# Kernel optimization log

Hardware: AMD Instinct MI355X
Metric: run time of the kernel (lower is better)

## Reference

```python
import jax, jax.numpy as jnp
import numpy as np
import itertools

D_MODEL = 1024
TEMP = 0.3


def _hypercube(n):
    # all 2^n corners of {-1,+1}^n, matching generate_hypercube(n)
    return jnp.asarray(np.array(list(itertools.product([-1.0, 1.0], repeat=n)), dtype=np.float32))


def setup_inputs() -> dict:
    key = jax.random.key(0)
    ks = jax.random.split(key, 12)
    B, T, D = 8, 4096, D_MODEL
    s = 0.02
    return {
        "x": jax.random.normal(ks[0], (B, T, D), dtype=jnp.float32),
        "codes_l1": _hypercube(3),   # (8, 3)
        "codes_l2": _hypercube(6),   # (64, 6)
        "w_to_l1": jax.random.normal(ks[1], (D, 3), dtype=jnp.float32) * s,
        "w_from_l1": jax.random.normal(ks[2], (3, D), dtype=jnp.float32) * s,
        "w_to_l2": jax.random.normal(ks[3], (D, 6), dtype=jnp.float32) * s,
        "w_from_l2": jax.random.normal(ks[4], (6, D), dtype=jnp.float32) * s,
        "w_to_l3u": jax.random.normal(ks[5], (D, 6), dtype=jnp.float32) * s,
        "w_to_l3l": jax.random.normal(ks[6], (D, 6), dtype=jnp.float32) * s,
        "w_from_l3": jax.random.normal(ks[7], (12, D), dtype=jnp.float32) * s,
        "w_gate": jax.random.normal(ks[8], (D, 3), dtype=jnp.float32) * s,
        "b_gate": jnp.zeros((3,), dtype=jnp.float32),
        "temp_l1": jnp.log(jnp.float32(TEMP)),
        "temp_l2": jnp.log(jnp.float32(TEMP * 0.7)),
        "temp_l3": jnp.log(jnp.float32(TEMP * 0.5)),
        "scale_l1": jnp.float32(0.1),
        "scale_l2": jnp.float32(0.05),
        "scale_l3": jnp.float32(0.02),
    }


def _soft_quantize(z, codes, temp_log):
    # z: (B, T, n); codes: (K, n) -> (B, T, n)
    temp = jnp.clip(jnp.exp(temp_log), 0.01, 5.0)
    # Euclidean cdist: (B, T, K)
    dists = jnp.sqrt(jnp.sum(jnp.square(z[..., None, :] - codes), axis=-1))
    weights = jax.nn.softmax(-dists / temp, axis=-1)
    return weights @ codes


def reference(x, codes_l1, codes_l2, w_to_l1, w_from_l1, w_to_l2, w_from_l2,
              w_to_l3u, w_to_l3l, w_from_l3, w_gate, b_gate,
              temp_l1, temp_l2, temp_l3, scale_l1, scale_l2, scale_l3):
    # gate uses detached x
    gate = jax.nn.softmax(jax.lax.stop_gradient(x) @ w_gate + b_gate, axis=-1)  # (B,T,3)

    # Level 1: Z2^3
    q1 = _soft_quantize(x @ w_to_l1, codes_l1, temp_l1)
    out_l1 = q1 @ w_from_l1

    # Level 2: Z2^6
    q2 = _soft_quantize(x @ w_to_l2, codes_l2, temp_l2)
    out_l2 = q2 @ w_from_l2

    # Level 3: Z2^12 = two Z2^6 halves
    q3u = _soft_quantize(x @ w_to_l3u, codes_l2, temp_l3)
    q3l = _soft_quantize(x @ w_to_l3l, codes_l2, temp_l3)
    out_l3 = jnp.concatenate([q3u, q3l], axis=-1) @ w_from_l3

    out = (gate[..., 0:1] * scale_l1 * out_l1
           + gate[..., 1:2] * scale_l2 * out_l2
           + gate[..., 2:3] * scale_l3 * out_l3)
    gate_means = jnp.mean(gate, axis=(0, 1))  # stats dict analogue: (3,)
    return x + out, gate_means
```

## Files before the change

### kernel.cpp

```cpp
#include <hip/hip_runtime.h>
#include <stdint.h>


#define DM 1024
#define TPB 64
#define OUT_OFF ((size_t)33554432)
#define NTOK 32768
#define NSLOT 32
#define WSA_OFF 32768

typedef float f32x4 __attribute__((ext_vector_type(4)));
typedef short bf16x8 __attribute__((ext_vector_type(8)));

typedef const __attribute__((address_space(1))) unsigned int* gas1_t;
typedef __attribute__((address_space(3))) unsigned int* las3_t;

__device__ __forceinline__ void gl_lds16(const void* g, void* l){
  __builtin_amdgcn_global_load_lds((gas1_t)g, (las3_t)l, 16, 0, 0);
}

__device__ __forceinline__ short f2bf(float f){
  unsigned u = __builtin_bit_cast(unsigned, f);
  unsigned r = u + 0x7fffu + ((u >> 16) & 1u);
  return (short)(r >> 16);
}

template<int NB>
__device__ __forceinline__ void softq(const float* z, float invt, float* q){
  constexpr int K = 1 << NB;
  float d[K];
  float dmin = 3.4e38f;
#pragma unroll
  for (int j = 0; j < K; ++j){
    float acc = 0.f;
#pragma unroll
    for (int i = 0; i < NB; ++i){
      float c = ((j >> (NB-1-i)) & 1) ? 1.f : -1.f;
      float t = z[i] - c;
      acc = fmaf(t, t, acc);
    }
    float dj = sqrtf(acc);
    d[j] = dj;
    dmin = fminf(dmin, dj);
  }
  float S = 0.f;
  float s1[NB];
#pragma unroll
  for (int i = 0; i < NB; ++i) s1[i] = 0.f;
#pragma unroll
  for (int j = 0; j < K; ++j){
    float wj = __expf((dmin - d[j]) * invt);
    S += wj;
#pragma unroll
    for (int i = 0; i < NB; ++i)
      if ((j >> (NB-1-i)) & 1) s1[i] += wj;
  }
  float rS = 1.f / S;
#pragma unroll
  for (int i = 0; i < NB; ++i) q[i] = 2.f * s1[i] * rS - 1.f;
}

__global__ __launch_bounds__(256) void pack_kernel(
    const float* __restrict__ w_to_l1,  const float* __restrict__ w_to_l2,
    const float* __restrict__ w_to_l3u, const float* __restrict__ w_to_l3l,
    const float* __restrict__ w_gate,
    const float* __restrict__ w_from_l1, const float* __restrict__ w_from_l2,
    const float* __restrict__ w_from_l3,
    short* __restrict__ wsF, float* __restrict__ wsA)
{
  int base = blockIdx.x*4096 + threadIdx.x*16;
#pragma unroll
  for (int q = 0; q < 16; ++q){
    int e = base + q;
    float v;
    if (e < 32768){
      int s  = e >> 10;
      int nf = (e >> 9) & 1;
      int ll = (e >> 3) & 63;
      int j  = e & 7;
      int k  = s*32 + ((ll >> 4) << 3) + j;
      int n  = nf*16 + (ll & 15);
      if      (n < 3)  v = w_gate  [k*3 + n];
      else if (n < 6)  v = w_to_l1 [k*3 + (n-3)];
      else if (n < 12) v = w_to_l2 [k*6 + (n-6)];
      else if (n < 18) v = w_to_l3u[k*6 + (n-12)];
      else if (n < 24) v = w_to_l3l[k*6 + (n-18)];
      else             v = 0.f;
    } else {
      int e2  = e - 32768;
      int f   = e2 / 384;
      int rem = e2 - f*384;
      int ll  = rem >> 3;
      int j   = e2 & 7;
      int k   = ((ll >> 4) << 3) + j;
      int dd  = f*16 + (ll & 15);
      if      (k < 3)  v = w_from_l1[k*DM + dd];
      else if (k < 9)  v = w_from_l2[(k-3)*DM + dd];
      else if (k < 21) v = w_from_l3[(k-9)*DM + dd];
      else             v = 0.f;
    }
    wsF[e] = f2bf(v);
  }
  if (blockIdx.x == 0){
    wsA[threadIdx.x]       = 0.f;
    wsA[threadIdx.x + 256] = 0.f;
  }
}

__global__ __launch_bounds__(256, 2) void hq8_kernel(
    const float* __restrict__ x, const short* __restrict__ wsF,
    const float* __restrict__ b_gate,
    const float* __restrict__ t1p, const float* __restrict__ t2p, const float* __restrict__ t3p,
    const float* __restrict__ s1p, const float* __restrict__ s2p, const float* __restrict__ s3p,
    float* __restrict__ wsA, float* __restrict__ out)
{
  __shared__ alignas(16) char smem[65536];

  const int tid  = threadIdx.x;
  const int l    = tid & 63;
  const int wv   = tid >> 6;
  const int kg   = l >> 4;
  const int ln16 = l & 15;
  const int tokBase = blockIdx.x * TPB + wv*16;

  char*  W  = smem + wv*16384;
  float* Cw = reinterpret_cast<float*>(W + 8192);
  float* Pw = reinterpret_cast<float*>(W + 12544);
  short* Vw = reinterpret_cast<short*>(W + 14720);

  const float invt1 = 1.f / fminf(fmaxf(__expf(t1p[0]), 0.01f), 5.0f);
  const float invt2 = 1.f / fminf(fmaxf(__expf(t2p[0]), 0.01f), 5.0f);
  const float invt3 = 1.f / fminf(fmaxf(__expf(t3p[0]), 0.01f), 5.0f);
  const float s1v = s1p[0], s2v = s2p[0], s3v = s3p[0];
  const float bg0 = b_gate[0], bg1 = b_gate[1], bg2 = b_gate[2];

  {
    f32x4 acc0 = {0.f,0.f,0.f,0.f}, acc1 = {0.f,0.f,0.f,0.f};
    const int lr0 = l >> 5;
    const int cbp = l & 31;
#pragma unroll
    for (int i = 0; i < 8; ++i){
      int lr = i*2 + lr0;
      gl_lds16(x + (size_t)(tokBase + lr)*DM + (cbp ^ (lr & 7))*4,
               W + i*1024 + l*16);
    }
#pragma unroll
    for (int t = 0; t < 8; ++t){
      const int buf = t & 1;
      bf16x8 bfr[8];
#pragma unroll
      for (int s2 = 0; s2 < 8; ++s2)
        bfr[s2] = *reinterpret_cast<const bf16x8*>(&wsF[(t*8 + s2)*512 + l*8]);
      __builtin_amdgcn_sched_barrier(0);
      if (t < 7){
#pragma unroll
        for (int i = 0; i < 8; ++i){
          int lr = i*2 + lr0;
          gl_lds16(x + (size_t)(tokBase + lr)*DM + (t+1)*128 + (cbp ^ (lr & 7))*4,
                   W + (buf^1)*8192 + i*1024 + l*16);
        }
        asm volatile("s_waitcnt vmcnt(8)" ::: "memory");
      } else {
        asm volatile("s_waitcnt vmcnt(0)" ::: "memory");
      }
      const char* abase = W + buf*8192 + ln16*512;
#pragma unroll
      for (int s = 0; s < 4; ++s){
        float4 xa = *reinterpret_cast<const float4*>(abase + ((s*8 + kg*2 + 0) ^ (ln16 & 7))*16);
        float4 xb = *reinterpret_cast<const float4*>(abase + ((s*8 + kg*2 + 1) ^ (ln16 & 7))*16);
        bf16x8 af;
        af[0]=f2bf(xa.x); af[1]=f2bf(xa.y); af[2]=f2bf(xa.z); af[3]=f2bf(xa.w);
        af[4]=f2bf(xb.x); af[5]=f2bf(xb.y); af[6]=f2bf(xb.z); af[7]=f2bf(xb.w);
        acc0 = __builtin_amdgcn_mfma_f32_16x16x32_bf16(af, bfr[s*2+0], acc0, 0, 0, 0);
        acc1 = __builtin_amdgcn_mfma_f32_16x16x32_bf16(af, bfr[s*2+1], acc1, 0, 0, 0);
      }
    }
#pragma unroll
    for (int r = 0; r < 4; ++r){
      int row = kg*4 + r;
      Pw[row*34 + ln16]      = acc0[r];
      Pw[row*34 + 16 + ln16] = acc1[r];
    }
  }

  const short* wsFC = wsF + 32768;
  bf16x8 bwc0={0,0,0,0,0,0,0,0}, bwc1=bwc0, bwc2=bwc0, bwc3=bwc0;
  {
#pragma unroll
    for (int j = 0; j < 4; ++j){
      int lr = j*4 + (l >> 4);
      gl_lds16(x + (size_t)(tokBase + lr)*DM + ((l & 15) ^ (lr & 7))*4,
               W + j*1024 + l*16);
    }
    if (kg < 3){
      bwc0 = *reinterpret_cast<const bf16x8*>(&wsFC[0*384 + l*8]);
      bwc1 = *reinterpret_cast<const bf16x8*>(&wsFC[1*384 + l*8]);
      bwc2 = *reinterpret_cast<const bf16x8*>(&wsFC[2*384 + l*8]);
      bwc3 = *reinterpret_cast<const bf16x8*>(&wsFC[3*384 + l*8]);
    }
#pragma unroll
    for (int j = 0; j < 4; ++j){
      int lr = j*4 + (l >> 4);
      gl_lds16(x + (size_t)(tokBase + lr)*DM + 64 + ((l & 15) ^ (lr & 7))*4,
               W + 4096 + j*1024 + l*16);
    }
  }

  float qv[6] = {0,0,0,0,0,0};
  float myscale = 0.f, g1s2v = 0.f, g2s3v = 0.f;
  float sg0 = 0.f, sg1 = 0.f, sg2 = 0.f;
  {
    const int t  = ln16;
    const int gi = kg;
    const int base = (gi == 3) ? 0 : 6 + gi*6;
    float z[6];
#pragma unroll
    for (int i = 0; i < 6; ++i) z[i] = Pw[t*34 + base + i];
    if (gi == 3){
      float g0l = z[0] + bg0;
      float g1l = z[1] + bg1;
      float g2l = z[2] + bg2;
      float m  = fmaxf(g0l, fmaxf(g1l, g2l));
      float e0 = __expf(g0l - m), e1 = __expf(g1l - m), e2 = __expf(g2l - m);
      float rs = 1.f / (e0 + e1 + e2);
      float g0 = e0*rs, g1 = e1*rs, g2 = e2*rs;
      myscale = g0 * s1v;
      g1s2v   = g1 * s2v;
      g2s3v   = g2 * s3v;
      float z1[3] = {z[3], z[4], z[5]};
      softq<3>(z1, invt1, qv);
      sg0 = g0; sg1 = g1; sg2 = g2;
#pragma unroll
      for (int mm = 1; mm < 16; mm <<= 1){
        sg0 += __shfl_xor(sg0, mm, 64);
        sg1 += __shfl_xor(sg1, mm, 64);
        sg2 += __shfl_xor(sg2, mm, 64);
      }
    } else {
      float invt = (gi == 0) ? invt2 : invt3;
      softq<6>(z, invt, qv);
    }
    float gs1 = __shfl(g1s2v, 48 + t, 64);
    float gs2 = __shfl(g2s3v, 48 + t, 64);
    if (gi == 3){
#pragma unroll
      for (int i = 0; i < 3; ++i) Vw[t*40 + i] = f2bf(myscale * qv[i]);
      Vw[t*40 + 21] = 0; Vw[t*40 + 22] = 0; Vw[t*40 + 23] = 0;
    } else {
      float sc = (gi == 0) ? gs1 : gs2;
      int voff = 3 + gi*6;
#pragma unroll
      for (int i = 0; i < 6; ++i) Vw[t*40 + voff + i] = f2bf(sc * qv[i]);
    }
  }

  bf16x8 aV = {0,0,0,0,0,0,0,0};
  if (kg < 3)
    aV = *reinterpret_cast<const bf16x8*>(&Vw[ln16*40 + kg*8]);
  const f32x4 z4 = {0.f,0.f,0.f,0.f};
  const int rl = l >> 2;
  const int cs = l & 3;

#pragma unroll
  for (int c = 0; c < 16; ++c){
    if (c == 0 || c == 15) asm volatile("s_waitcnt vmcnt(4)" ::: "memory");
    else                   asm volatile("s_waitcnt vmcnt(8)" ::: "memory");
    __builtin_amdgcn_sched_barrier(0);
    {
      f32x4 d0 = __builtin_amdgcn_mfma_f32_16x16x32_bf16(aV, bwc0, z4, 0, 0, 0);
      f32x4 d1 = __builtin_amdgcn_mfma_f32_16x16x32_bf16(aV, bwc1, z4, 0, 0, 0);
      f32x4 d2 = __builtin_amdgcn_mfma_f32_16x16x32_bf16(aV, bwc2, z4, 0, 0, 0);
      f32x4 d3 = __builtin_amdgcn_mfma_f32_16x16x32_bf16(aV, bwc3, z4, 0, 0, 0);
#pragma unroll
      for (int r = 0; r < 4; ++r){
        int rowb = (kg*4 + r)*68;
        Cw[rowb +  0 + ln16] = d0[r];
        Cw[rowb + 16 + ln16] = d1[r];
        Cw[rowb + 32 + ln16] = d2[r];
        Cw[rowb + 48 + ln16] = d3[r];
      }
    }
    __builtin_amdgcn_sched_barrier(0);
    bf16x8 bwn0 = bwc0, bwn1 = bwc1, bwn2 = bwc2, bwn3 = bwc3;
    if (c < 15 && kg < 3){
      bwn0 = *reinterpret_cast<const bf16x8*>(&wsFC[((c+1)*4+0)*384 + l*8]);
      bwn1 = *reinterpret_cast<const bf16x8*>(&wsFC[((c+1)*4+1)*384 + l*8]);
      bwn2 = *reinterpret_cast<const bf16x8*>(&wsFC[((c+1)*4+2)*384 + l*8]);
      bwn3 = *reinterpret_cast<const bf16x8*>(&wsFC[((c+1)*4+3)*384 + l*8]);
    }
    __builtin_amdgcn_sched_barrier(0);
    asm volatile("s_waitcnt lgkmcnt(0)" ::: "memory");
    __builtin_amdgcn_sched_barrier(0);
#pragma unroll
    for (int q = 0; q < 4; ++q){
      int bi = cs + 4*q;
      f32x4 xv = *reinterpret_cast<const f32x4*>(
          W + (c & 1)*4096 + rl*256 + ((bi ^ (rl & 7)))*16);
      f32x4 cv = *reinterpret_cast<const f32x4*>(&Cw[rl*68 + bi*4]);
      f32x4 ov = xv + cv;
      *reinterpret_cast<f32x4*>(&out[(size_t)(tokBase + rl)*DM + c*64 + bi*4]) = ov;
    }
    __builtin_amdgcn_sched_barrier(0);
    if (c < 14){
#pragma unroll
      for (int j = 0; j < 4; ++j){
        int lr = j*4 + (l >> 4);
        gl_lds16(x + (size_t)(tokBase + lr)*DM + (c+2)*64 + ((l & 15) ^ (lr & 7))*4,
                 W + (c & 1)*4096 + j*1024 + l*16);
      }
    }
    bwc0 = bwn0; bwc1 = bwn1; bwc2 = bwn2; bwc3 = bwn3;
  }

  if (l == 48){
    float* slot = wsA + ((blockIdx.x*4 + wv) & (NSLOT-1))*16;
    atomicAdd(slot + 0, sg0);
    atomicAdd(slot + 1, sg1);
    atomicAdd(slot + 2, sg2);
  }
}

__global__ void finalize_kernel(const float* __restrict__ wsA, float* __restrict__ out){
  if (threadIdx.x < 3){
    float s = 0.f;
    for (int j = 0; j < NSLOT; ++j) s += wsA[j*16 + threadIdx.x];
    out[OUT_OFF + threadIdx.x] = s * (1.f / (float)NTOK);
  }
}

extern "C" void kernel_launch(void* const* d_in, const int* in_sizes, int n_in,
                              void* d_out, int out_size, void* d_ws, size_t ws_size,
                              hipStream_t stream){
  (void)in_sizes; (void)n_in; (void)ws_size; (void)out_size;
  const float* x         = (const float*)d_in[0];
  const float* w_to_l1   = (const float*)d_in[3];
  const float* w_from_l1 = (const float*)d_in[4];
  const float* w_to_l2   = (const float*)d_in[5];
  const float* w_from_l2 = (const float*)d_in[6];
  const float* w_to_l3u  = (const float*)d_in[7];
  const float* w_to_l3l  = (const float*)d_in[8];
  const float* w_from_l3 = (const float*)d_in[9];
  const float* w_gate    = (const float*)d_in[10];
  const float* b_gate    = (const float*)d_in[11];
  const float* t1 = (const float*)d_in[12];
  const float* t2 = (const float*)d_in[13];
  const float* t3 = (const float*)d_in[14];
  const float* s1 = (const float*)d_in[15];
  const float* s2 = (const float*)d_in[16];
  const float* s3 = (const float*)d_in[17];
  float* out  = (float*)d_out;
  short* wsF  = (short*)d_ws;
  float* wsA  = (float*)d_ws + WSA_OFF;

  pack_kernel<<<dim3(14), dim3(256), 0, stream>>>(
      w_to_l1, w_to_l2, w_to_l3u, w_to_l3l, w_gate,
      w_from_l1, w_from_l2, w_from_l3, wsF, wsA);
  hq8_kernel<<<dim3(512), dim3(256), 0, stream>>>(
      x, wsF, b_gate, t1, t2, t3, s1, s2, s3, wsA, out);
  finalize_kernel<<<dim3(1), dim3(64), 0, stream>>>(wsA, out);
}
```

Measured before the change: 81.03 us.

## Process two token tiles per wave, overlapping second tile's projection with first's epilogue

Each wave now handles two 16-token tiles, 32 tokens in all, so a block covers 128 tokens and the grid shrinks to 256 blocks. The second tile's x loads and projection MFMAs are interleaved into the first tile's output epilogue, hiding the projection phase behind the output writes. The epilogue now reads x straight from global into registers instead of staging it through LDS. LDS use rises to 96KB and launch bounds drop to one block per CU, which lowers occupancy. The second tile's epilogue has no prefetch pipelining.

```diff
diff --git a/kernel.cpp b/kernel.cpp
--- a/kernel.cpp
+++ b/kernel.cpp
@@ -3,7 +3,6 @@
 
 
 #define DM 1024
-#define TPB 64
 #define OUT_OFF ((size_t)33554432)
 #define NTOK 32768
 #define NSLOT 32
@@ -107,42 +106,151 @@
   }
 }
 
-__global__ __launch_bounds__(256, 2) void hq8_kernel(
+__device__ __forceinline__ void quant16(const float* Pw, short* Vw, int l,
+    float invt1, float invt2, float invt3, float s1v, float s2v, float s3v,
+    float bg0, float bg1, float bg2, float& sg0, float& sg1, float& sg2)
+{
+  const int t  = l & 15;
+  const int gi = l >> 4;
+  const int base = (gi == 3) ? 0 : 6 + gi*6;
+  float z[6];
+#pragma unroll
+  for (int i = 0; i < 6; ++i) z[i] = Pw[t*34 + base + i];
+  float qv[6] = {0,0,0,0,0,0};
+  float myscale = 0.f, g1s2v = 0.f, g2s3v = 0.f;
+  if (gi == 3){
+    float g0l = z[0] + bg0;
+    float g1l = z[1] + bg1;
+    float g2l = z[2] + bg2;
+    float m  = fmaxf(g0l, fmaxf(g1l, g2l));
+    float e0 = __expf(g0l - m), e1 = __expf(g1l - m), e2 = __expf(g2l - m);
+    float rs = 1.f / (e0 + e1 + e2);
+    float g0 = e0*rs, g1 = e1*rs, g2 = e2*rs;
+    myscale = g0 * s1v;
+    g1s2v   = g1 * s2v;
+    g2s3v   = g2 * s3v;
+    float z1[3] = {z[3], z[4], z[5]};
+    softq<3>(z1, invt1, qv);
+    float a0 = g0, a1 = g1, a2 = g2;
+#pragma unroll
+    for (int mm = 1; mm < 16; mm <<= 1){
+      a0 += __shfl_xor(a0, mm, 64);
+      a1 += __shfl_xor(a1, mm, 64);
+      a2 += __shfl_xor(a2, mm, 64);
+    }
+    sg0 += a0; sg1 += a1; sg2 += a2;
+  } else {
+    float invt = (gi == 0) ? invt2 : invt3;
+    softq<6>(z, invt, qv);
+  }
+  float gs1 = __shfl(g1s2v, 48 + t, 64);
+  float gs2 = __shfl(g2s3v, 48 + t, 64);
+  if (gi == 3){
+#pragma unroll
+    for (int i = 0; i < 3; ++i) Vw[t*40 + i] = f2bf(myscale * qv[i]);
+    Vw[t*40 + 21] = 0; Vw[t*40 + 22] = 0; Vw[t*40 + 23] = 0;
+  } else {
+    float sc = (gi == 0) ? gs1 : gs2;
+    int voff = 3 + gi*6;
+#pragma unroll
+    for (int i = 0; i < 6; ++i) Vw[t*40 + voff + i] = f2bf(sc * qv[i]);
+  }
+}
+
+struct EpiL { bf16x8 b0, b1, b2, b3; f32x4 x0, x1, x2, x3; };
+
+__device__ __forceinline__ EpiL epi_load(int c, const short* wsFC,
+                                         const float* xT, int l, int kg,
+                                         int rl, int cs){
+  EpiL L;
+  bf16x8 z8 = {0,0,0,0,0,0,0,0};
+  L.b0 = z8; L.b1 = z8; L.b2 = z8; L.b3 = z8;
+  if (kg < 3){
+    L.b0 = *reinterpret_cast<const bf16x8*>(&wsFC[(c*4+0)*384 + l*8]);
+    L.b1 = *reinterpret_cast<const bf16x8*>(&wsFC[(c*4+1)*384 + l*8]);
+    L.b2 = *reinterpret_cast<const bf16x8*>(&wsFC[(c*4+2)*384 + l*8]);
+    L.b3 = *reinterpret_cast<const bf16x8*>(&wsFC[(c*4+3)*384 + l*8]);
+  }
+  const float* xr = xT + (size_t)rl*DM + c*64 + cs*4;
+  L.x0 = *reinterpret_cast<const f32x4*>(xr);
+  L.x1 = *reinterpret_cast<const f32x4*>(xr + 16);
+  L.x2 = *reinterpret_cast<const f32x4*>(xr + 32);
+  L.x3 = *reinterpret_cast<const f32x4*>(xr + 48);
+  return L;
+}
+
+__device__ __forceinline__ void epi_store(int c, const EpiL& L, bf16x8 aV,
+    float* Cw, float* outT, int kg, int ln16, int rl, int cs){
+  const f32x4 z4 = {0.f,0.f,0.f,0.f};
+  f32x4 d0 = __builtin_amdgcn_mfma_f32_16x16x32_bf16(aV, L.b0, z4, 0, 0, 0);
+  f32x4 d1 = __builtin_amdgcn_mfma_f32_16x16x32_bf16(aV, L.b1, z4, 0, 0, 0);
+  f32x4 d2 = __builtin_amdgcn_mfma_f32_16x16x32_bf16(aV, L.b2, z4, 0, 0, 0);
+  f32x4 d3 = __builtin_amdgcn_mfma_f32_16x16x32_bf16(aV, L.b3, z4, 0, 0, 0);
+#pragma unroll
+  for (int r = 0; r < 4; ++r){
+    int rowb = (kg*4 + r)*68;
+    Cw[rowb +  0 + ln16] = d0[r];
+    Cw[rowb + 16 + ln16] = d1[r];
+    Cw[rowb + 32 + ln16] = d2[r];
+    Cw[rowb + 48 + ln16] = d3[r];
+  }
+  const float* cr = &Cw[rl*68 + cs*4];
+  f32x4 c0 = *reinterpret_cast<const f32x4*>(cr);
+  f32x4 c1 = *reinterpret_cast<const f32x4*>(cr + 16);
+  f32x4 c2 = *reinterpret_cast<const f32x4*>(cr + 32);
+  f32x4 c3 = *reinterpret_cast<const f32x4*>(cr + 48);
+  float* orow = outT + (size_t)rl*DM + c*64 + cs*4;
+  *reinterpret_cast<f32x4*>(orow)      = L.x0 + c0;
+  *reinterpret_cast<f32x4*>(orow + 16) = L.x1 + c1;
+  *reinterpret_cast<f32x4*>(orow + 32) = L.x2 + c2;
+  *reinterpret_cast<f32x4*>(orow + 48) = L.x3 + c3;
+}
+
+__global__ __launch_bounds__(256, 1) void hq9_kernel(
     const float* __restrict__ x, const short* __restrict__ wsF,
     const float* __restrict__ b_gate,
     const float* __restrict__ t1p, const float* __restrict__ t2p, const float* __restrict__ t3p,
     const float* __restrict__ s1p, const float* __restrict__ s2p, const float* __restrict__ s3p,
     float* __restrict__ wsA, float* __restrict__ out)
 {
-  __shared__ alignas(16) char smem[65536];
+  __shared__ alignas(16) char smem[98304];
 
   const int tid  = threadIdx.x;
   const int l    = tid & 63;
   const int wv   = tid >> 6;
   const int kg   = l >> 4;
   const int ln16 = l & 15;
-  const int tokBase = blockIdx.x * TPB + wv*16;
-
-  char*  W  = smem + wv*16384;
-  float* Cw = reinterpret_cast<float*>(W + 8192);
-  float* Pw = reinterpret_cast<float*>(W + 12544);
-  short* Vw = reinterpret_cast<short*>(W + 14720);
+  const int rl   = l >> 2;
+  const int cs   = l & 3;
+  const int lr0  = l >> 5;
+  const int cbp  = l & 31;
+
+  const size_t tokA = (size_t)blockIdx.x*128 + wv*32;
+  char*  W  = smem + wv*24576;
+  float* Cw = reinterpret_cast<float*>(W + 16384);
+  float* Pw = reinterpret_cast<float*>(W + 20736);
+  short* Vw = reinterpret_cast<short*>(W + 22912);
+
+  const float* xA   = x + tokA*DM;
+  const float* xB   = xA + (size_t)16*DM;
+  float*       outA = out + tokA*DM;
+  float*       outB = outA + (size_t)16*DM;
+  const short* wsFC = wsF + 32768;
 
   const float invt1 = 1.f / fminf(fmaxf(__expf(t1p[0]), 0.01f), 5.0f);
   const float invt2 = 1.f / fminf(fmaxf(__expf(t2p[0]), 0.01f), 5.0f);
   const float invt3 = 1.f / fminf(fmaxf(__expf(t3p[0]), 0.01f), 5.0f);
   const float s1v = s1p[0], s2v = s2p[0], s3v = s3p[0];
   const float bg0 = b_gate[0], bg1 = b_gate[1], bg2 = b_gate[2];
+  float sg0 = 0.f, sg1 = 0.f, sg2 = 0.f;
+  const bf16x8 z8 = {0,0,0,0,0,0,0,0};
 
   {
     f32x4 acc0 = {0.f,0.f,0.f,0.f}, acc1 = {0.f,0.f,0.f,0.f};
-    const int lr0 = l >> 5;
-    const int cbp = l & 31;
 #pragma unroll
     for (int i = 0; i < 8; ++i){
       int lr = i*2 + lr0;
-      gl_lds16(x + (size_t)(tokBase + lr)*DM + (cbp ^ (lr & 7))*4,
-               W + i*1024 + l*16);
+      gl_lds16(xA + (size_t)lr*DM + (cbp ^ (lr & 7))*4, W + i*1024 + l*16);
     }
 #pragma unroll
     for (int t = 0; t < 8; ++t){
@@ -156,13 +264,14 @@
 #pragma unroll
         for (int i = 0; i < 8; ++i){
           int lr = i*2 + lr0;
-          gl_lds16(x + (size_t)(tokBase + lr)*DM + (t+1)*128 + (cbp ^ (lr & 7))*4,
+          gl_lds16(xA + (size_t)lr*DM + (t+1)*128 + (cbp ^ (lr & 7))*4,
                    W + (buf^1)*8192 + i*1024 + l*16);
         }
         asm volatile("s_waitcnt vmcnt(8)" ::: "memory");
       } else {
         asm volatile("s_waitcnt vmcnt(0)" ::: "memory");
       }
+      __builtin_amdgcn_sched_barrier(0);
       const char* abase = W + buf*8192 + ln16*512;
 #pragma unroll
       for (int s = 0; s < 4; ++s){
@@ -183,133 +292,73 @@
     }
   }
 
-  const short* wsFC = wsF + 32768;
-  bf16x8 bwc0={0,0,0,0,0,0,0,0}, bwc1=bwc0, bwc2=bwc0, bwc3=bwc0;
-  {
-#pragma unroll
-    for (int j = 0; j < 4; ++j){
-      int lr = j*4 + (l >> 4);
-      gl_lds16(x + (size_t)(tokBase + lr)*DM + ((l & 15) ^ (lr & 7))*4,
-               W + j*1024 + l*16);
-    }
-    if (kg < 3){
-      bwc0 = *reinterpret_cast<const bf16x8*>(&wsFC[0*384 + l*8]);
-      bwc1 = *reinterpret_cast<const bf16x8*>(&wsFC[1*384 + l*8]);
-      bwc2 = *reinterpret_cast<const bf16x8*>(&wsFC[2*384 + l*8]);
-      bwc3 = *reinterpret_cast<const bf16x8*>(&wsFC[3*384 + l*8]);
-    }
-#pragma unroll
-    for (int j = 0; j < 4; ++j){
-      int lr = j*4 + (l >> 4);
-      gl_lds16(x + (size_t)(tokBase + lr)*DM + 64 + ((l & 15) ^ (lr & 7))*4,
-               W + 4096 + j*1024 + l*16);
-    }
-  }
-
-  float qv[6] = {0,0,0,0,0,0};
-  float myscale = 0.f, g1s2v = 0.f, g2s3v = 0.f;
-  float sg0 = 0.f, sg1 = 0.f, sg2 = 0.f;
-  {
-    const int t  = ln16;
-    const int gi = kg;
-    const int base = (gi == 3) ? 0 : 6 + gi*6;
-    float z[6];
-#pragma unroll
-    for (int i = 0; i < 6; ++i) z[i] = Pw[t*34 + base + i];
-    if (gi == 3){
-      float g0l = z[0] + bg0;
-      float g1l = z[1] + bg1;
-      float g2l = z[2] + bg2;
-      float m  = fmaxf(g0l, fmaxf(g1l, g2l));
-      float e0 = __expf(g0l - m), e1 = __expf(g1l - m), e2 = __expf(g2l - m);
-      float rs = 1.f / (e0 + e1 + e2);
-      float g0 = e0*rs, g1 = e1*rs, g2 = e2*rs;
-      myscale = g0 * s1v;
-      g1s2v   = g1 * s2v;
-      g2s3v   = g2 * s3v;
-      float z1[3] = {z[3], z[4], z[5]};
-      softq<3>(z1, invt1, qv);
-      sg0 = g0; sg1 = g1; sg2 = g2;
-#pragma unroll
-      for (int mm = 1; mm < 16; mm <<= 1){
-        sg0 += __shfl_xor(sg0, mm, 64);
-        sg1 += __shfl_xor(sg1, mm, 64);
-        sg2 += __shfl_xor(sg2, mm, 64);
+  quant16(Pw, Vw, l, invt1, invt2, invt3, s1v, s2v, s3v, bg0, bg1, bg2, sg0, sg1, sg2);
+  bf16x8 aVA = z8;
+  if (kg < 3) aVA = *reinterpret_cast<const bf16x8*>(&Vw[ln16*40 + kg*8]);
+
+  EpiL L = epi_load(0, wsFC, xA, l, kg, rl, cs);
+  __builtin_amdgcn_sched_barrier(0);
+#pragma unroll
+  for (int i = 0; i < 8; ++i){
+    int lr = i*2 + lr0;
+    gl_lds16(xB + (size_t)lr*DM + (cbp ^ (lr & 7))*4, W + i*1024 + l*16);
+  }
+  __builtin_amdgcn_sched_barrier(0);
+
+  f32x4 accB0 = {0.f,0.f,0.f,0.f}, accB1 = {0.f,0.f,0.f,0.f};
+#pragma unroll
+  for (int c = 0; c < 16; ++c){
+    if (c & 1){
+      asm volatile("s_waitcnt vmcnt(4)" ::: "memory");
+      __builtin_amdgcn_sched_barrier(0);
+      const int k = (c-1) >> 1;
+      bf16x8 bfr[8];
+#pragma unroll
+      for (int s2 = 0; s2 < 8; ++s2)
+        bfr[s2] = *reinterpret_cast<const bf16x8*>(&wsF[(k*8 + s2)*512 + l*8]);
+      const char* abase = W + (k&1)*8192 + ln16*512;
+#pragma unroll
+      for (int s = 0; s < 4; ++s){
+        float4 xa = *reinterpret_cast<const float4*>(abase + ((s*8 + kg*2 + 0) ^ (ln16 & 7))*16);
+        float4 xb = *reinterpret_cast<const float4*>(abase + ((s*8 + kg*2 + 1) ^ (ln16 & 7))*16);
+        bf16x8 af;
+        af[0]=f2bf(xa.x); af[1]=f2bf(xa.y); af[2]=f2bf(xa.z); af[3]=f2bf(xa.w);
+        af[4]=f2bf(xb.x); af[5]=f2bf(xb.y); af[6]=f2bf(xb.z); af[7]=f2bf(xb.w);
+        accB0 = __builtin_amdgcn_mfma_f32_16x16x32_bf16(af, bfr[s*2+0], accB0, 0, 0, 0);
+        accB1 = __builtin_amdgcn_mfma_f32_16x16x32_bf16(af, bfr[s*2+1], accB1, 0, 0, 0);
       }
-    } else {
-      float invt = (gi == 0) ? invt2 : invt3;
-      softq<6>(z, invt, qv);
-    }
-    float gs1 = __shfl(g1s2v, 48 + t, 64);
-    float gs2 = __shfl(g2s3v, 48 + t, 64);
-    if (gi == 3){
-#pragma unroll
-      for (int i = 0; i < 3; ++i) Vw[t*40 + i] = f2bf(myscale * qv[i]);
-      Vw[t*40 + 21] = 0; Vw[t*40 + 22] = 0; Vw[t*40 + 23] = 0;
-    } else {
-      float sc = (gi == 0) ? gs1 : gs2;
-      int voff = 3 + gi*6;
-#pragma unroll
-      for (int i = 0; i < 6; ++i) Vw[t*40 + voff + i] = f2bf(sc * qv[i]);
-    }
-  }
-
-  bf16x8 aV = {0,0,0,0,0,0,0,0};
-  if (kg < 3)
-    aV = *reinterpret_cast<const bf16x8*>(&Vw[ln16*40 + kg*8]);
-  const f32x4 z4 = {0.f,0.f,0.f,0.f};
-  const int rl = l >> 2;
-  const int cs = l & 3;
+      __builtin_amdgcn_sched_barrier(0);
+      L = epi_load(c, wsFC, xA, l, kg, rl, cs);
+      __builtin_amdgcn_sched_barrier(0);
+    } else if (c >= 2){
+      L = epi_load(c, wsFC, xA, l, kg, rl, cs);
+      __builtin_amdgcn_sched_barrier(0);
+      const int k2 = c >> 1;
+#pragma unroll
+      for (int i = 0; i < 8; ++i){
+        int lr = i*2 + lr0;
+        gl_lds16(xB + (size_t)lr*DM + k2*128 + (cbp ^ (lr & 7))*4,
+                 W + (k2&1)*8192 + i*1024 + l*16);
+      }
+      __builtin_amdgcn_sched_barrier(0);
+    }
+    epi_store(c, L, aVA, Cw, outA, kg, ln16, rl, cs);
+  }
+
+#pragma unroll
+  for (int r = 0; r < 4; ++r){
+    int row = kg*4 + r;
+    Pw[row*34 + ln16]      = accB0[r];
+    Pw[row*34 + 16 + ln16] = accB1[r];
+  }
+  quant16(Pw, Vw, l, invt1, invt2, invt3, s1v, s2v, s3v, bg0, bg1, bg2, sg0, sg1, sg2);
+  bf16x8 aVB = z8;
+  if (kg < 3) aVB = *reinterpret_cast<const bf16x8*>(&Vw[ln16*40 + kg*8]);
 
 #pragma unroll
   for (int c = 0; c < 16; ++c){
-    if (c == 0 || c == 15) asm volatile("s_waitcnt vmcnt(4)" ::: "memory");
-    else                   asm volatile("s_waitcnt vmcnt(8)" ::: "memory");
-    __builtin_amdgcn_sched_barrier(0);
-    {
-      f32x4 d0 = __builtin_amdgcn_mfma_f32_16x16x32_bf16(aV, bwc0, z4, 0, 0, 0);
-      f32x4 d1 = __builtin_amdgcn_mfma_f32_16x16x32_bf16(aV, bwc1, z4, 0, 0, 0);
-      f32x4 d2 = __builtin_amdgcn_mfma_f32_16x16x32_bf16(aV, bwc2, z4, 0, 0, 0);
-      f32x4 d3 = __builtin_amdgcn_mfma_f32_16x16x32_bf16(aV, bwc3, z4, 0, 0, 0);
-#pragma unroll
-      for (int r = 0; r < 4; ++r){
-        int rowb = (kg*4 + r)*68;
-        Cw[rowb +  0 + ln16] = d0[r];
-        Cw[rowb + 16 + ln16] = d1[r];
-        Cw[rowb + 32 + ln16] = d2[r];
-        Cw[rowb + 48 + ln16] = d3[r];
-      }
-    }
-    __builtin_amdgcn_sched_barrier(0);
-    bf16x8 bwn0 = bwc0, bwn1 = bwc1, bwn2 = bwc2, bwn3 = bwc3;
-    if (c < 15 && kg < 3){
-      bwn0 = *reinterpret_cast<const bf16x8*>(&wsFC[((c+1)*4+0)*384 + l*8]);
-      bwn1 = *reinterpret_cast<const bf16x8*>(&wsFC[((c+1)*4+1)*384 + l*8]);
-      bwn2 = *reinterpret_cast<const bf16x8*>(&wsFC[((c+1)*4+2)*384 + l*8]);
-      bwn3 = *reinterpret_cast<const bf16x8*>(&wsFC[((c+1)*4+3)*384 + l*8]);
-    }
-    __builtin_amdgcn_sched_barrier(0);
-    asm volatile("s_waitcnt lgkmcnt(0)" ::: "memory");
-    __builtin_amdgcn_sched_barrier(0);
-#pragma unroll
-    for (int q = 0; q < 4; ++q){
-      int bi = cs + 4*q;
-      f32x4 xv = *reinterpret_cast<const f32x4*>(
-          W + (c & 1)*4096 + rl*256 + ((bi ^ (rl & 7)))*16);
-      f32x4 cv = *reinterpret_cast<const f32x4*>(&Cw[rl*68 + bi*4]);
-      f32x4 ov = xv + cv;
-      *reinterpret_cast<f32x4*>(&out[(size_t)(tokBase + rl)*DM + c*64 + bi*4]) = ov;
-    }
-    __builtin_amdgcn_sched_barrier(0);
-    if (c < 14){
-#pragma unroll
-      for (int j = 0; j < 4; ++j){
-        int lr = j*4 + (l >> 4);
-        gl_lds16(x + (size_t)(tokBase + lr)*DM + (c+2)*64 + ((l & 15) ^ (lr & 7))*4,
-                 W + (c & 1)*4096 + j*1024 + l*16);
-      }
-    }
-    bwc0 = bwn0; bwc1 = bwn1; bwc2 = bwn2; bwc3 = bwn3;
+    EpiL Lb = epi_load(c, wsFC, xB, l, kg, rl, cs);
+    epi_store(c, Lb, aVB, Cw, outB, kg, ln16, rl, cs);
   }
 
   if (l == 48){
@@ -355,7 +404,7 @@
   pack_kernel<<<dim3(14), dim3(256), 0, stream>>>(
       w_to_l1, w_to_l2, w_to_l3u, w_to_l3l, w_gate,
       w_from_l1, w_from_l2, w_from_l3, wsF, wsA);
-  hq8_kernel<<<dim3(512), dim3(256), 0, stream>>>(
+  hq9_kernel<<<dim3(256), dim3(256), 0, stream>>>(
       x, wsF, b_gate, t1, t2, t3, s1, s2, s3, wsA, out);
   finalize_kernel<<<dim3(1), dim3(64), 0, stream>>>(wsA, out);
 }
```

Result: slower. 130.5 us (+61.0%).

## Warp-specialize kernel into projection producers and quantize/output consumers

Applied to the files above, without the earlier changes.

The fused kernel is split into warp roles within 512-thread blocks of 128 tokens. Four producer waves each compute a K-quarter of the down-projection via MFMA and write partials to double-buffered LDS. Four consumer waves reduce those partials, run the gate softmax and soft quantization, then do the up-projection and residual write for their column quarter. They hand off through block barriers, with consumer from-weights held in registers and x re-read directly from global memory. The aim is to overlap the reduction GEMM with the output stage, at the cost of more LDS per block (about 103 KB), barrier coupling, and a second global read of x.

```diff
diff --git a/kernel.cpp b/kernel.cpp
--- a/kernel.cpp
+++ b/kernel.cpp
@@ -3,11 +3,14 @@
 
 
 #define DM 1024
-#define TPB 64
 #define OUT_OFF ((size_t)33554432)
 #define NTOK 32768
 #define NSLOT 32
 #define WSA_OFF 32768
+
+#define POFF 65536
+#define VOFF 82944
+#define COFF 88064
 
 typedef float f32x4 __attribute__((ext_vector_type(4)));
 typedef short bf16x8 __attribute__((ext_vector_type(8)));
@@ -107,216 +110,230 @@
   }
 }
 
-__global__ __launch_bounds__(256, 2) void hq8_kernel(
+__global__ __launch_bounds__(512, 2) void hq11_kernel(
     const float* __restrict__ x, const short* __restrict__ wsF,
     const float* __restrict__ b_gate,
     const float* __restrict__ t1p, const float* __restrict__ t2p, const float* __restrict__ t3p,
     const float* __restrict__ s1p, const float* __restrict__ s2p, const float* __restrict__ s3p,
     float* __restrict__ wsA, float* __restrict__ out)
 {
-  __shared__ alignas(16) char smem[65536];
+  __shared__ alignas(16) char smem[105472];
 
   const int tid  = threadIdx.x;
   const int l    = tid & 63;
-  const int wv   = tid >> 6;
+  const int wid  = tid >> 6;
   const int kg   = l >> 4;
   const int ln16 = l & 15;
-  const int tokBase = blockIdx.x * TPB + wv*16;
-
-  char*  W  = smem + wv*16384;
-  float* Cw = reinterpret_cast<float*>(W + 8192);
-  float* Pw = reinterpret_cast<float*>(W + 12544);
-  short* Vw = reinterpret_cast<short*>(W + 14720);
-
-  const float invt1 = 1.f / fminf(fmaxf(__expf(t1p[0]), 0.01f), 5.0f);
-  const float invt2 = 1.f / fminf(fmaxf(__expf(t2p[0]), 0.01f), 5.0f);
-  const float invt3 = 1.f / fminf(fmaxf(__expf(t3p[0]), 0.01f), 5.0f);
-  const float s1v = s1p[0], s2v = s2p[0], s3v = s3p[0];
-  const float bg0 = b_gate[0], bg1 = b_gate[1], bg2 = b_gate[2];
-
-  {
-    f32x4 acc0 = {0.f,0.f,0.f,0.f}, acc1 = {0.f,0.f,0.f,0.f};
+  const size_t tokB = (size_t)blockIdx.x * 128;
+  const short* wsFC = wsF + 32768;
+  const bf16x8 z8 = {0,0,0,0,0,0,0,0};
+
+  if (wid < 4){
+    const int pw  = wid;
+    char* stg = smem + pw*16384;
     const int lr0 = l >> 5;
     const int cbp = l & 31;
+
 #pragma unroll
     for (int i = 0; i < 8; ++i){
       int lr = i*2 + lr0;
-      gl_lds16(x + (size_t)(tokBase + lr)*DM + (cbp ^ (lr & 7))*4,
-               W + i*1024 + l*16);
-    }
-#pragma unroll
-    for (int t = 0; t < 8; ++t){
-      const int buf = t & 1;
-      bf16x8 bfr[8];
-#pragma unroll
-      for (int s2 = 0; s2 < 8; ++s2)
-        bfr[s2] = *reinterpret_cast<const bf16x8*>(&wsF[(t*8 + s2)*512 + l*8]);
+      gl_lds16(x + (tokB + lr)*DM + pw*256 + (cbp ^ (lr & 7))*4,
+               stg + i*1024 + l*16);
+    }
+
+#pragma unroll
+    for (int s = 0; s < 8; ++s){
+      f32x4 acc0 = {0.f,0.f,0.f,0.f}, acc1 = {0.f,0.f,0.f,0.f};
+#pragma unroll
+      for (int ci = 0; ci < 2; ++ci){
+        const int n = s*2 + ci;
+        bf16x8 bfr[8];
+#pragma unroll
+        for (int s2 = 0; s2 < 8; ++s2)
+          bfr[s2] = *reinterpret_cast<const bf16x8*>(
+              &wsF[(size_t)(pw*16 + ci*8 + s2)*512 + l*8]);
+        __builtin_amdgcn_sched_barrier(0);
+        if (n < 15){
+          const int np = n + 1, sp = np >> 1, cip = np & 1;
+#pragma unroll
+          for (int i = 0; i < 8; ++i){
+            int lr = i*2 + lr0;
+            gl_lds16(x + (tokB + sp*16 + lr)*DM + pw*256 + cip*128 + (cbp ^ (lr & 7))*4,
+                     stg + (np & 1)*8192 + i*1024 + l*16);
+          }
+          asm volatile("s_waitcnt vmcnt(8)" ::: "memory");
+        } else {
+          asm volatile("s_waitcnt vmcnt(0)" ::: "memory");
+        }
+        __builtin_amdgcn_sched_barrier(0);
+        const char* ab = stg + (n & 1)*8192 + ln16*512;
+#pragma unroll
+        for (int s2 = 0; s2 < 4; ++s2){
+          float4 xa = *reinterpret_cast<const float4*>(ab + (size_t)((s2*8 + kg*2 + 0) ^ (ln16 & 7))*16);
+          float4 xb = *reinterpret_cast<const float4*>(ab + (size_t)((s2*8 + kg*2 + 1) ^ (ln16 & 7))*16);
+          bf16x8 af;
+          af[0]=f2bf(xa.x); af[1]=f2bf(xa.y); af[2]=f2bf(xa.z); af[3]=f2bf(xa.w);
+          af[4]=f2bf(xb.x); af[5]=f2bf(xb.y); af[6]=f2bf(xb.z); af[7]=f2bf(xb.w);
+          acc0 = __builtin_amdgcn_mfma_f32_16x16x32_bf16(af, bfr[s2*2+0], acc0, 0, 0, 0);
+          acc1 = __builtin_amdgcn_mfma_f32_16x16x32_bf16(af, bfr[s2*2+1], acc1, 0, 0, 0);
+        }
+      }
+      float* Pp = reinterpret_cast<float*>(smem + POFF + (s & 1)*8704) + pw*544;
+#pragma unroll
+      for (int r = 0; r < 4; ++r){
+        Pp[(kg*4 + r)*34 + ln16]      = acc0[r];
+        Pp[(kg*4 + r)*34 + 16 + ln16] = acc1[r];
+      }
+      asm volatile("s_waitcnt lgkmcnt(0)" ::: "memory");
       __builtin_amdgcn_sched_barrier(0);
-      if (t < 7){
-#pragma unroll
-        for (int i = 0; i < 8; ++i){
-          int lr = i*2 + lr0;
-          gl_lds16(x + (size_t)(tokBase + lr)*DM + (t+1)*128 + (cbp ^ (lr & 7))*4,
-                   W + (buf^1)*8192 + i*1024 + l*16);
-        }
-        asm volatile("s_waitcnt vmcnt(8)" ::: "memory");
-      } else {
-        asm volatile("s_waitcnt vmcnt(0)" ::: "memory");
-      }
-      const char* abase = W + buf*8192 + ln16*512;
-#pragma unroll
-      for (int s = 0; s < 4; ++s){
-        float4 xa = *reinterpret_cast<const float4*>(abase + ((s*8 + kg*2 + 0) ^ (ln16 & 7))*16);
-        float4 xb = *reinterpret_cast<const float4*>(abase + ((s*8 + kg*2 + 1) ^ (ln16 & 7))*16);
-        bf16x8 af;
-        af[0]=f2bf(xa.x); af[1]=f2bf(xa.y); af[2]=f2bf(xa.z); af[3]=f2bf(xa.w);
-        af[4]=f2bf(xb.x); af[5]=f2bf(xb.y); af[6]=f2bf(xb.z); af[7]=f2bf(xb.w);
-        acc0 = __builtin_amdgcn_mfma_f32_16x16x32_bf16(af, bfr[s*2+0], acc0, 0, 0, 0);
-        acc1 = __builtin_amdgcn_mfma_f32_16x16x32_bf16(af, bfr[s*2+1], acc1, 0, 0, 0);
-      }
-    }
-#pragma unroll
-    for (int r = 0; r < 4; ++r){
-      int row = kg*4 + r;
-      Pw[row*34 + ln16]      = acc0[r];
-      Pw[row*34 + 16 + ln16] = acc1[r];
-    }
-  }
-
-  const short* wsFC = wsF + 32768;
-  bf16x8 bwc0={0,0,0,0,0,0,0,0}, bwc1=bwc0, bwc2=bwc0, bwc3=bwc0;
-  {
-#pragma unroll
-    for (int j = 0; j < 4; ++j){
-      int lr = j*4 + (l >> 4);
-      gl_lds16(x + (size_t)(tokBase + lr)*DM + ((l & 15) ^ (lr & 7))*4,
-               W + j*1024 + l*16);
-    }
-    if (kg < 3){
-      bwc0 = *reinterpret_cast<const bf16x8*>(&wsFC[0*384 + l*8]);
-      bwc1 = *reinterpret_cast<const bf16x8*>(&wsFC[1*384 + l*8]);
-      bwc2 = *reinterpret_cast<const bf16x8*>(&wsFC[2*384 + l*8]);
-      bwc3 = *reinterpret_cast<const bf16x8*>(&wsFC[3*384 + l*8]);
-    }
-#pragma unroll
-    for (int j = 0; j < 4; ++j){
-      int lr = j*4 + (l >> 4);
-      gl_lds16(x + (size_t)(tokBase + lr)*DM + 64 + ((l & 15) ^ (lr & 7))*4,
-               W + 4096 + j*1024 + l*16);
-    }
-  }
-
-  float qv[6] = {0,0,0,0,0,0};
-  float myscale = 0.f, g1s2v = 0.f, g2s3v = 0.f;
-  float sg0 = 0.f, sg1 = 0.f, sg2 = 0.f;
-  {
-    const int t  = ln16;
-    const int gi = kg;
-    const int base = (gi == 3) ? 0 : 6 + gi*6;
-    float z[6];
-#pragma unroll
-    for (int i = 0; i < 6; ++i) z[i] = Pw[t*34 + base + i];
-    if (gi == 3){
-      float g0l = z[0] + bg0;
-      float g1l = z[1] + bg1;
-      float g2l = z[2] + bg2;
-      float m  = fmaxf(g0l, fmaxf(g1l, g2l));
-      float e0 = __expf(g0l - m), e1 = __expf(g1l - m), e2 = __expf(g2l - m);
-      float rs = 1.f / (e0 + e1 + e2);
-      float g0 = e0*rs, g1 = e1*rs, g2 = e2*rs;
-      myscale = g0 * s1v;
-      g1s2v   = g1 * s2v;
-      g2s3v   = g2 * s3v;
-      float z1[3] = {z[3], z[4], z[5]};
-      softq<3>(z1, invt1, qv);
-      sg0 = g0; sg1 = g1; sg2 = g2;
-#pragma unroll
-      for (int mm = 1; mm < 16; mm <<= 1){
-        sg0 += __shfl_xor(sg0, mm, 64);
-        sg1 += __shfl_xor(sg1, mm, 64);
-        sg2 += __shfl_xor(sg2, mm, 64);
-      }
-    } else {
-      float invt = (gi == 0) ? invt2 : invt3;
-      softq<6>(z, invt, qv);
-    }
-    float gs1 = __shfl(g1s2v, 48 + t, 64);
-    float gs2 = __shfl(g2s3v, 48 + t, 64);
-    if (gi == 3){
-#pragma unroll
-      for (int i = 0; i < 3; ++i) Vw[t*40 + i] = f2bf(myscale * qv[i]);
-      Vw[t*40 + 21] = 0; Vw[t*40 + 22] = 0; Vw[t*40 + 23] = 0;
-    } else {
-      float sc = (gi == 0) ? gs1 : gs2;
-      int voff = 3 + gi*6;
-#pragma unroll
-      for (int i = 0; i < 6; ++i) Vw[t*40 + voff + i] = f2bf(sc * qv[i]);
-    }
-  }
-
-  bf16x8 aV = {0,0,0,0,0,0,0,0};
-  if (kg < 3)
-    aV = *reinterpret_cast<const bf16x8*>(&Vw[ln16*40 + kg*8]);
-  const f32x4 z4 = {0.f,0.f,0.f,0.f};
-  const int rl = l >> 2;
-  const int cs = l & 3;
-
-#pragma unroll
-  for (int c = 0; c < 16; ++c){
-    if (c == 0 || c == 15) asm volatile("s_waitcnt vmcnt(4)" ::: "memory");
-    else                   asm volatile("s_waitcnt vmcnt(8)" ::: "memory");
-    __builtin_amdgcn_sched_barrier(0);
-    {
-      f32x4 d0 = __builtin_amdgcn_mfma_f32_16x16x32_bf16(aV, bwc0, z4, 0, 0, 0);
-      f32x4 d1 = __builtin_amdgcn_mfma_f32_16x16x32_bf16(aV, bwc1, z4, 0, 0, 0);
-      f32x4 d2 = __builtin_amdgcn_mfma_f32_16x16x32_bf16(aV, bwc2, z4, 0, 0, 0);
-      f32x4 d3 = __builtin_amdgcn_mfma_f32_16x16x32_bf16(aV, bwc3, z4, 0, 0, 0);
-#pragma unroll
-      for (int r = 0; r < 4; ++r){
-        int rowb = (kg*4 + r)*68;
-        Cw[rowb +  0 + ln16] = d0[r];
-        Cw[rowb + 16 + ln16] = d1[r];
-        Cw[rowb + 32 + ln16] = d2[r];
-        Cw[rowb + 48 + ln16] = d3[r];
-      }
-    }
-    __builtin_amdgcn_sched_barrier(0);
-    bf16x8 bwn0 = bwc0, bwn1 = bwc1, bwn2 = bwc2, bwn3 = bwc3;
-    if (c < 15 && kg < 3){
-      bwn0 = *reinterpret_cast<const bf16x8*>(&wsFC[((c+1)*4+0)*384 + l*8]);
-      bwn1 = *reinterpret_cast<const bf16x8*>(&wsFC[((c+1)*4+1)*384 + l*8]);
-      bwn2 = *reinterpret_cast<const bf16x8*>(&wsFC[((c+1)*4+2)*384 + l*8]);
-      bwn3 = *reinterpret_cast<const bf16x8*>(&wsFC[((c+1)*4+3)*384 + l*8]);
-    }
-    __builtin_amdgcn_sched_barrier(0);
-    asm volatile("s_waitcnt lgkmcnt(0)" ::: "memory");
-    __builtin_amdgcn_sched_barrier(0);
-#pragma unroll
-    for (int q = 0; q < 4; ++q){
-      int bi = cs + 4*q;
-      f32x4 xv = *reinterpret_cast<const f32x4*>(
-          W + (c & 1)*4096 + rl*256 + ((bi ^ (rl & 7)))*16);
-      f32x4 cv = *reinterpret_cast<const f32x4*>(&Cw[rl*68 + bi*4]);
-      f32x4 ov = xv + cv;
-      *reinterpret_cast<f32x4*>(&out[(size_t)(tokBase + rl)*DM + c*64 + bi*4]) = ov;
-    }
-    __builtin_amdgcn_sched_barrier(0);
-    if (c < 14){
-#pragma unroll
-      for (int j = 0; j < 4; ++j){
-        int lr = j*4 + (l >> 4);
-        gl_lds16(x + (size_t)(tokBase + lr)*DM + (c+2)*64 + ((l & 15) ^ (lr & 7))*4,
-                 W + (c & 1)*4096 + j*1024 + l*16);
-      }
-    }
-    bwc0 = bwn0; bwc1 = bwn1; bwc2 = bwn2; bwc3 = bwn3;
-  }
-
-  if (l == 48){
-    float* slot = wsA + ((blockIdx.x*4 + wv) & (NSLOT-1))*16;
-    atomicAdd(slot + 0, sg0);
-    atomicAdd(slot + 1, sg1);
-    atomicAdd(slot + 2, sg2);
+      __builtin_amdgcn_s_barrier();
+      __builtin_amdgcn_sched_barrier(0);
+    }
+  } else {
+    const int cw = wid - 4;
+    short* Vw = reinterpret_cast<short*>(smem + VOFF + cw*1280);
+    float* Cw = reinterpret_cast<float*>(smem + COFF + cw*4352);
+    const int rl = l >> 2;
+    const int cs = l & 3;
+
+    const float invt1 = 1.f / fminf(fmaxf(__expf(t1p[0]), 0.01f), 5.0f);
+    const float invt2 = 1.f / fminf(fmaxf(__expf(t2p[0]), 0.01f), 5.0f);
+    const float invt3 = 1.f / fminf(fmaxf(__expf(t3p[0]), 0.01f), 5.0f);
+    const float s1v = s1p[0], s2v = s2p[0], s3v = s3p[0];
+    const float bg0 = b_gate[0], bg1 = b_gate[1], bg2 = b_gate[2];
+    float sg0 = 0.f, sg1 = 0.f, sg2 = 0.f;
+
+    bf16x8 bw[4][4];
+#pragma unroll
+    for (int j = 0; j < 4; ++j)
+#pragma unroll
+      for (int ff = 0; ff < 4; ++ff){
+        bw[j][ff] = z8;
+        if (kg < 3)
+          bw[j][ff] = *reinterpret_cast<const bf16x8*>(
+              &wsFC[(size_t)((cw*4 + j)*4 + ff)*384 + l*8]);
+      }
+
+    f32x4 xc0, xc1, xc2, xc3;
+#pragma unroll
+    for (int s = 0; s <= 8; ++s){
+      if (s > 0){
+        const int t = s - 1;
+        if (t == 0){
+          const float* xr = x + (tokB + rl)*DM + cw*256 + cs*4;
+          xc0 = *reinterpret_cast<const f32x4*>(xr);
+          xc1 = *reinterpret_cast<const f32x4*>(xr + 16);
+          xc2 = *reinterpret_cast<const f32x4*>(xr + 32);
+          xc3 = *reinterpret_cast<const f32x4*>(xr + 48);
+        }
+        {
+          const int tq = ln16;
+          const int gi = kg;
+          const int base = (gi == 3) ? 0 : 6 + gi*6;
+          const float* P0 = reinterpret_cast<const float*>(smem + POFF + (t & 1)*8704);
+          float z[6];
+#pragma unroll
+          for (int i = 0; i < 6; ++i){
+            int idx = tq*34 + base + i;
+            z[i] = P0[idx] + P0[544 + idx] + P0[1088 + idx] + P0[1632 + idx];
+          }
+          float qv[6] = {0,0,0,0,0,0};
+          float myscale = 0.f, g1s2v = 0.f, g2s3v = 0.f;
+          if (gi == 3){
+            float g0l = z[0] + bg0;
+            float g1l = z[1] + bg1;
+            float g2l = z[2] + bg2;
+            float m  = fmaxf(g0l, fmaxf(g1l, g2l));
+            float e0 = __expf(g0l - m), e1 = __expf(g1l - m), e2 = __expf(g2l - m);
+            float rs = 1.f / (e0 + e1 + e2);
+            float g0 = e0*rs, g1 = e1*rs, g2 = e2*rs;
+            myscale = g0 * s1v;
+            g1s2v   = g1 * s2v;
+            g2s3v   = g2 * s3v;
+            float z1[3] = {z[3], z[4], z[5]};
+            softq<3>(z1, invt1, qv);
+            float a0 = g0, a1 = g1, a2 = g2;
+#pragma unroll
+            for (int mm = 1; mm < 16; mm <<= 1){
+              a0 += __shfl_xor(a0, mm, 64);
+              a1 += __shfl_xor(a1, mm, 64);
+              a2 += __shfl_xor(a2, mm, 64);
+            }
+            sg0 += a0; sg1 += a1; sg2 += a2;
+          } else {
+            float invt = (gi == 0) ? invt2 : invt3;
+            softq<6>(z, invt, qv);
+          }
+          float gs1 = __shfl(g1s2v, 48 + tq, 64);
+          float gs2 = __shfl(g2s3v, 48 + tq, 64);
+          if (gi == 3){
+#pragma unroll
+            for (int i = 0; i < 3; ++i) Vw[tq*40 + i] = f2bf(myscale * qv[i]);
+            Vw[tq*40 + 21] = 0; Vw[tq*40 + 22] = 0; Vw[tq*40 + 23] = 0;
+          } else {
+            float sc = (gi == 0) ? gs1 : gs2;
+            int voff = 3 + gi*6;
+#pragma unroll
+            for (int i = 0; i < 6; ++i) Vw[tq*40 + voff + i] = f2bf(sc * qv[i]);
+          }
+        }
+        bf16x8 aV = z8;
+        if (kg < 3) aV = *reinterpret_cast<const bf16x8*>(&Vw[ln16*40 + kg*8]);
+
+#pragma unroll
+        for (int j = 0; j < 4; ++j){
+          f32x4 xn0 = xc0, xn1 = xc1, xn2 = xc2, xn3 = xc3;
+          if (!(t == 7 && j == 3)){
+            const int tn = (j < 3) ? t : t + 1;
+            const int jn = (j < 3) ? j + 1 : 0;
+            const float* xr = x + (tokB + tn*16 + rl)*DM + cw*256 + jn*64 + cs*4;
+            xn0 = *reinterpret_cast<const f32x4*>(xr);
+            xn1 = *reinterpret_cast<const f32x4*>(xr + 16);
+            xn2 = *reinterpret_cast<const f32x4*>(xr + 32);
+            xn3 = *reinterpret_cast<const f32x4*>(xr + 48);
+          }
+          __builtin_amdgcn_sched_barrier(0);
+          const f32x4 zz = {0.f,0.f,0.f,0.f};
+          f32x4 d0 = __builtin_amdgcn_mfma_f32_16x16x32_bf16(aV, bw[j][0], zz, 0, 0, 0);
+          f32x4 d1 = __builtin_amdgcn_mfma_f32_16x16x32_bf16(aV, bw[j][1], zz, 0, 0, 0);
+          f32x4 d2 = __builtin_amdgcn_mfma_f32_16x16x32_bf16(aV, bw[j][2], zz, 0, 0, 0);
+          f32x4 d3 = __builtin_amdgcn_mfma_f32_16x16x32_bf16(aV, bw[j][3], zz, 0, 0, 0);
+#pragma unroll
+          for (int r = 0; r < 4; ++r){
+            int rb = (kg*4 + r)*68;
+            Cw[rb +  0 + ln16] = d0[r];
+            Cw[rb + 16 + ln16] = d1[r];
+            Cw[rb + 32 + ln16] = d2[r];
+            Cw[rb + 48 + ln16] = d3[r];
+          }
+          __builtin_amdgcn_sched_barrier(0);
+          f32x4 c0 = *reinterpret_cast<const f32x4*>(&Cw[rl*68 + cs*4]);
+          f32x4 c1 = *reinterpret_cast<const f32x4*>(&Cw[rl*68 + cs*4 + 16]);
+          f32x4 c2 = *reinterpret_cast<const f32x4*>(&Cw[rl*68 + cs*4 + 32]);
+          f32x4 c3 = *reinterpret_cast<const f32x4*>(&Cw[rl*68 + cs*4 + 48]);
+          float* orow = out + (tokB + t*16 + rl)*DM + cw*256 + j*64 + cs*4;
+          *reinterpret_cast<f32x4*>(orow)      = xc0 + c0;
+          *reinterpret_cast<f32x4*>(orow + 16) = xc1 + c1;
+          *reinterpret_cast<f32x4*>(orow + 32) = xc2 + c2;
+          *reinterpret_cast<f32x4*>(orow + 48) = xc3 + c3;
+          __builtin_amdgcn_sched_barrier(0);
+          xc0 = xn0; xc1 = xn1; xc2 = xn2; xc3 = xn3;
+        }
+      }
+      if (s < 8){
+        asm volatile("s_waitcnt lgkmcnt(0)" ::: "memory");
+        __builtin_amdgcn_sched_barrier(0);
+        __builtin_amdgcn_s_barrier();
+        __builtin_amdgcn_sched_barrier(0);
+      }
+    }
+
+    if (cw == 0 && l == 48){
+      float* slot = wsA + (blockIdx.x & (NSLOT-1))*16;
+      atomicAdd(slot + 0, sg0);
+      atomicAdd(slot + 1, sg1);
+      atomicAdd(slot + 2, sg2);
+    }
   }
 }
 
@@ -355,7 +372,7 @@
   pack_kernel<<<dim3(14), dim3(256), 0, stream>>>(
       w_to_l1, w_to_l2, w_to_l3u, w_to_l3l, w_gate,
       w_from_l1, w_from_l2, w_from_l3, wsF, wsA);
-  hq8_kernel<<<dim3(512), dim3(256), 0, stream>>>(
+  hq11_kernel<<<dim3(256), dim3(512), 0, stream>>>(
       x, wsF, b_gate, t1, t2, t3, s1, s2, s3, wsA, out);
   finalize_kernel<<<dim3(1), dim3(64), 0, stream>>>(wsA, out);
 }
```

Result: slower. 240.1 us (+196.3%).
